# Optimization experiments

Hardware: AMD Instinct MI355X
Metric: run time of the kernel (lower is better)

Reference implementation:

```python
import jax, jax.numpy as jnp
import numpy as np

N, D_IN, D_OUT, Q_DIM = 4096, 256, 256, 64


def _xavier(key, shape):
    fan_in, fan_out = shape[-2], shape[-1]
    bound = float(np.sqrt(6.0 / (fan_in + fan_out)))
    return jax.random.uniform(key, shape, jnp.float32, -bound, bound)


def setup_inputs() -> dict:
    key = jax.random.key(0)
    k_x, k_q, k_w, k_b = jax.random.split(key, 4)
    x = jax.random.normal(k_x, (N, D_IN), jnp.float32)
    query_vectors = jax.random.normal(k_q, (N, Q_DIM), jnp.float32)
    W_1 = _xavier(k_w, (Q_DIM, D_IN, D_OUT))  # xavier over last two dims (matches torch on 3D)
    b_1 = _xavier(k_b, (Q_DIM, D_OUT))
    return {"x": x, "query_vectors": query_vectors, "W_1": W_1, "b_1": b_1}


def reference(x, query_vectors, W_1, b_1):
    # Per-sample dynamic weight: W[n] = sum_d q[n,d] * W_1[d]; then x[n] @ W[n] + q[n] @ b_1.
    # Fused single contraction avoids materializing the [n, i, o] tensor; same math.
    out = jnp.einsum('ni,nd,dio->no', x, query_vectors, W_1)
    out = out + query_vectors @ b_1
    return out
```

## Files before the change

kernel.cpp:

```cpp
#include <hip/hip_runtime.h>
#include <stdint.h>


typedef _Float16 f16;
typedef f16 f16x8 __attribute__((ext_vector_type(8)));
typedef float f32x16 __attribute__((ext_vector_type(16)));

#define QDIM 64

#define XFRAG(DST, PTR)                                      \
  do {                                                       \
    float4 a_ = *(const float4*)(PTR);                       \
    float4 b_ = *(const float4*)((PTR) + 4);                 \
    f16x8 h_;                                                \
    h_[0] = (f16)a_.x; h_[1] = (f16)a_.y; h_[2] = (f16)a_.z; \
    h_[3] = (f16)a_.w; h_[4] = (f16)b_.x; h_[5] = (f16)b_.y; \
    h_[6] = (f16)b_.z; h_[7] = (f16)b_.w;                    \
    DST = h_;                                                \
  } while (0)

__global__ __launch_bounds__(256) void prep(const float* __restrict__ W,
                                            const float* __restrict__ B1,
                                            const float* __restrict__ X,
                                            f16* __restrict__ Wt,
                                            f16* __restrict__ Xt,
                                            f16* __restrict__ Bt) {
  const int b = blockIdx.x, t = threadIdx.x;
  if (b < 512) {
    const int d = b >> 3, grp = b & 7;
#pragma unroll
    for (int r = 0; r < 4; ++r) {
      const int ib = (grp << 2) + r;
      const float* src = W + ((size_t)d * 256 + ((size_t)ib << 3)) * 256 + t;
      f16x8 h;
#pragma unroll
      for (int j = 0; j < 8; ++j) h[j] = (f16)src[(size_t)j << 8];
      const int nc = t >> 5, c = t & 31, ic = ib >> 1, hb = ib & 1;
      *(f16x8*)((char*)Wt + ((((size_t)nc * 64 + d) * 16 + ic) << 10) +
                (hb << 9) + (c << 4)) = h;
    }
  } else if (b < 576) {
    const int mb = b - 512;
#pragma unroll
    for (int rep = 0; rep < 8; ++rep) {
      const int u = (rep << 8) + t;
      const int row = u & 63, ish = u >> 6;
      const float* src = X + ((size_t)((mb << 6) + row)) * 256 + (ish << 3);
      f16x8 h;
      XFRAG(h, src);
      *(f16x8*)((char*)Xt + ((((size_t)mb * 16 + (ish >> 1)) * 2 + (ish & 1)) << 10) +
                (row << 4)) = h;
    }
  } else {
#pragma unroll
    for (int kb = 0; kb < 8; ++kb) {
      const float* src = B1 + ((size_t)kb << 3) * 256 + t;
      f16x8 h;
#pragma unroll
      for (int j = 0; j < 8; ++j) h[j] = (f16)src[(size_t)j << 8];
      *(f16x8*)((char*)Bt + (((size_t)(t >> 5) * 4 + (kb >> 1)) << 10) +
                ((kb & 1) << 9) + ((t & 31) << 4)) = h;
    }
  }
}

#define LOADX(D, IC)                                             \
  do {                                                           \
    D[0] = *(const f16x8*)(xb + ((size_t)(IC) << 11));           \
    D[1] = *(const f16x8*)(xb + ((size_t)(IC) << 11) + 512);     \
  } while (0)

#define FULL16(XF, ICN)                                                          \
  do {                                                                          \
    _Pragma("unroll")                                                           \
    for (int dq = 0; dq < 16; ++dq) {                                           \
      f16x8 wfr = Wr[dq];                                                       \
      Wr[dq] = *(const f16x8*)(wl + (((size_t)dq * 16 + (ICN)) << 10));         \
      f16x8 a0 = XF[0] * qr0[dq];                                               \
      acc0[dq & 1] = __builtin_amdgcn_mfma_f32_32x32x16_f16(                    \
          a0, wfr, acc0[dq & 1], 0, 0, 0);                                      \
      f16x8 a1 = XF[1] * qr1[dq];                                               \
      acc1[dq & 1] = __builtin_amdgcn_mfma_f32_32x32x16_f16(                    \
          a1, wfr, acc1[dq & 1], 0, 0, 0);                                      \
    }                                                                           \
  } while (0)

__global__ __launch_bounds__(256, 2) void mlp_main(const float* __restrict__ Q,
                                                   const f16* __restrict__ Wt,
                                                   const f16* __restrict__ Xt,
                                                   const f16* __restrict__ Bt,
                                                   float* __restrict__ out) {
  __shared__ __align__(16) float red[4][64][36];

  const int bid = blockIdx.x;
  const int nc = bid & 7;
  const int mb = bid >> 3;
  const int t = threadIdx.x;
  const int w = t >> 6;
  const int l = t & 63;
  const int l31 = l & 31;
  const int hf = l >> 5;

  const char* wl = (const char*)Wt + (((size_t)(nc * 64 + (w << 4))) << 14) +
                   (hf << 9) + (l31 << 4);
  const char* xb = (const char*)Xt + ((size_t)mb << 15) + (hf << 10) + (l31 << 4);

  f16 qr0[16], qr1[16];
  {
    const float* qp0 = Q + ((size_t)((mb << 6) + l31)) * QDIM + (w << 4);
    const float* qp1 = qp0 + (size_t)32 * QDIM;
#pragma unroll
    for (int g = 0; g < 4; ++g) {
      float4 v0 = *(const float4*)(qp0 + (g << 2));
      float4 v1 = *(const float4*)(qp1 + (g << 2));
      qr0[g * 4 + 0] = (f16)v0.x; qr0[g * 4 + 1] = (f16)v0.y;
      qr0[g * 4 + 2] = (f16)v0.z; qr0[g * 4 + 3] = (f16)v0.w;
      qr1[g * 4 + 0] = (f16)v1.x; qr1[g * 4 + 1] = (f16)v1.y;
      qr1[g * 4 + 2] = (f16)v1.z; qr1[g * 4 + 3] = (f16)v1.w;
    }
  }

  f32x16 acc0[2], acc1[2];
#pragma unroll
  for (int p = 0; p < 2; ++p)
#pragma unroll
    for (int r = 0; r < 16; ++r) { acc0[p][r] = 0.f; acc1[p][r] = 0.f; }

  f16x8 Wr[16], xfA[2], xfB[2];

  const int icoff = (mb & 7) << 1;

  LOADX(xfA, icoff);
#pragma unroll
  for (int dq = 0; dq < 16; ++dq)
    Wr[dq] = *(const f16x8*)(wl + (((size_t)dq * 16 + icoff) << 10));

  for (int ic2 = 0; ic2 < 8; ++ic2) {
    const int o  = ((ic2 << 1) + 1 + icoff) & 15;
    const int n2 = ((ic2 << 1) + 2 + icoff) & 15;
    LOADX(xfB, o);
    FULL16(xfA, o);
    LOADX(xfA, n2);
    FULL16(xfB, n2);
  }

#pragma unroll
  for (int r = 0; r < 16; ++r) {
    acc0[0][r] += acc0[1][r];
    acc1[0][r] += acc1[1][r];
  }

  if (w == 0) {
#pragma unroll
    for (int kc = 0; kc < 4; ++kc) {
      f16x8 bf = *(const f16x8*)((const char*)Bt +
          (((size_t)nc * 4 + kc) << 10) + (hf << 9) + (l31 << 4));
      f16x8 q0, q1;
      XFRAG(q0, Q + ((size_t)((mb << 6) + l31)) * QDIM + (kc << 4) + (hf << 3));
      XFRAG(q1, Q + ((size_t)((mb << 6) + 32 + l31)) * QDIM + (kc << 4) + (hf << 3));
      acc0[0] = __builtin_amdgcn_mfma_f32_32x32x16_f16(q0, bf, acc0[0], 0, 0, 0);
      acc1[0] = __builtin_amdgcn_mfma_f32_32x32x16_f16(q1, bf, acc1[0], 0, 0, 0);
    }
  }

#pragma unroll
  for (int r = 0; r < 16; ++r) {
    const int row0 = (r & 3) + ((r >> 2) << 3) + (hf << 2);
    red[w][row0][l31] = acc0[0][r];
    red[w][32 + row0][l31] = acc1[0][r];
  }
  __syncthreads();

  const int row = t >> 2;
  const int cq = (t & 3) << 3;
  float s[8];
#pragma unroll
  for (int j = 0; j < 8; ++j) s[j] = 0.f;
#pragma unroll
  for (int wq = 0; wq < 4; ++wq) {
    const float* rp = &red[wq][row][cq];
    float4 v0 = *(const float4*)rp;
    float4 v1 = *(const float4*)(rp + 4);
    s[0] += v0.x; s[1] += v0.y; s[2] += v0.z; s[3] += v0.w;
    s[4] += v1.x; s[5] += v1.y; s[6] += v1.z; s[7] += v1.w;
  }
  float4 o0 = {s[0], s[1], s[2], s[3]};
  float4 o1 = {s[4], s[5], s[6], s[7]};
  float* op = out + ((size_t)((mb << 6) + row)) * 256 + (nc << 5) + cq;
  *(float4*)op = o0;
  *(float4*)(op + 4) = o1;
}

extern "C" void kernel_launch(void* const* d_in, const int* in_sizes, int n_in,
                              void* d_out, int out_size, void* d_ws, size_t ws_size,
                              hipStream_t stream) {
  (void)in_sizes; (void)n_in; (void)out_size; (void)ws_size;
  const float* x  = (const float*)d_in[0];
  const float* q  = (const float*)d_in[1];
  const float* W1 = (const float*)d_in[2];
  const float* b1 = (const float*)d_in[3];
  float* out = (float*)d_out;

  f16* Wt = (f16*)d_ws;
  f16* Bt = (f16*)((char*)d_ws + ((size_t)8 << 20));
  f16* Xt = (f16*)((char*)d_ws + ((size_t)8 << 20) + 32768);

  prep<<<577, 256, 0, stream>>>(W1, b1, x, Wt, Xt, Bt);
  mlp_main<<<512, 256, 0, stream>>>(q, Wt, Xt, Bt, out);
}
```

Before: 120.6 us.

## Halve rows per block, double grid and occupancy; vectorize W prep loads

The main kernel now processes 32 rows per block instead of 64, launching 1024 blocks with a launch bound allowing 4 blocks per SM. The W register buffer is halved to 8 fragments, with a two-phase rotating prefetch over the 16 q-dimension slices, to cut register pressure and raise occupancy. The prep kernel now reads W with float4 loads per thread and transposes in registers to improve coalescing. In exchange, each W fragment loaded from memory is reused across half as many rows, doubling total W traffic from L2.

After: 133.1 us. 1.1x slower.

```diff
diff --git a/kernel.cpp b/kernel.cpp
--- a/kernel.cpp
+++ b/kernel.cpp
@@ -28,15 +28,24 @@
   const int b = blockIdx.x, t = threadIdx.x;
   if (b < 512) {
     const int d = b >> 3, grp = b & 7;
+    const int ibL = t >> 6;
+    const int ib = (grp << 2) + ibL;
+    const int o0 = (t & 63) << 2;
+    const int ic = ib >> 1, hb = ib & 1;
+    float v[32];
 #pragma unroll
-    for (int r = 0; r < 4; ++r) {
-      const int ib = (grp << 2) + r;
-      const float* src = W + ((size_t)d * 256 + ((size_t)ib << 3)) * 256 + t;
+    for (int j = 0; j < 8; ++j) {
+      float4 f = *(const float4*)(W + ((size_t)d * 256 + (ib << 3) + j) * 256 + o0);
+      v[j * 4 + 0] = f.x; v[j * 4 + 1] = f.y;
+      v[j * 4 + 2] = f.z; v[j * 4 + 3] = f.w;
+    }
+#pragma unroll
+    for (int oo = 0; oo < 4; ++oo) {
+      const int o = o0 + oo, ncb = o >> 5, c = o & 31;
       f16x8 h;
 #pragma unroll
-      for (int j = 0; j < 8; ++j) h[j] = (f16)src[(size_t)j << 8];
-      const int nc = t >> 5, c = t & 31, ic = ib >> 1, hb = ib & 1;
-      *(f16x8*)((char*)Wt + ((((size_t)nc * 64 + d) * 16 + ic) << 10) +
+      for (int j = 0; j < 8; ++j) h[j] = (f16)v[j * 4 + oo];
+      *(f16x8*)((char*)Wt + ((((size_t)ncb * 64 + d) * 16 + ic) << 10) +
                 (hb << 9) + (c << 4)) = h;
     }
   } else if (b < 576) {
@@ -64,33 +73,12 @@
   }
 }
 
-#define LOADX(D, IC)                                             \
-  do {                                                           \
-    D[0] = *(const f16x8*)(xb + ((size_t)(IC) << 11));           \
-    D[1] = *(const f16x8*)(xb + ((size_t)(IC) << 11) + 512);     \
-  } while (0)
-
-#define FULL16(XF, ICN)                                                          \
-  do {                                                                          \
-    _Pragma("unroll")                                                           \
-    for (int dq = 0; dq < 16; ++dq) {                                           \
-      f16x8 wfr = Wr[dq];                                                       \
-      Wr[dq] = *(const f16x8*)(wl + (((size_t)dq * 16 + (ICN)) << 10));         \
-      f16x8 a0 = XF[0] * qr0[dq];                                               \
-      acc0[dq & 1] = __builtin_amdgcn_mfma_f32_32x32x16_f16(                    \
-          a0, wfr, acc0[dq & 1], 0, 0, 0);                                      \
-      f16x8 a1 = XF[1] * qr1[dq];                                               \
-      acc1[dq & 1] = __builtin_amdgcn_mfma_f32_32x32x16_f16(                    \
-          a1, wfr, acc1[dq & 1], 0, 0, 0);                                      \
-    }                                                                           \
-  } while (0)
-
-__global__ __launch_bounds__(256, 2) void mlp_main(const float* __restrict__ Q,
+__global__ __launch_bounds__(256, 4) void mlp_main(const float* __restrict__ Q,
                                                    const f16* __restrict__ Wt,
                                                    const f16* __restrict__ Xt,
                                                    const f16* __restrict__ Bt,
                                                    float* __restrict__ out) {
-  __shared__ __align__(16) float red[4][64][36];
+  __shared__ __align__(16) float red[4][32][36];
 
   const int bid = blockIdx.x;
   const int nc = bid & 7;
@@ -103,92 +91,86 @@
 
   const char* wl = (const char*)Wt + (((size_t)(nc * 64 + (w << 4))) << 14) +
                    (hf << 9) + (l31 << 4);
-  const char* xb = (const char*)Xt + ((size_t)mb << 15) + (hf << 10) + (l31 << 4);
+  const char* xb = (const char*)Xt + ((size_t)(mb >> 1) << 15) + (hf << 10) +
+                   ((size_t)(((mb & 1) << 5) + l31) << 4);
 
-  f16 qr0[16], qr1[16];
+  f16 qr[16];
   {
-    const float* qp0 = Q + ((size_t)((mb << 6) + l31)) * QDIM + (w << 4);
-    const float* qp1 = qp0 + (size_t)32 * QDIM;
+    const float* qp = Q + ((size_t)((mb << 5) + l31)) * QDIM + (w << 4);
 #pragma unroll
     for (int g = 0; g < 4; ++g) {
-      float4 v0 = *(const float4*)(qp0 + (g << 2));
-      float4 v1 = *(const float4*)(qp1 + (g << 2));
-      qr0[g * 4 + 0] = (f16)v0.x; qr0[g * 4 + 1] = (f16)v0.y;
-      qr0[g * 4 + 2] = (f16)v0.z; qr0[g * 4 + 3] = (f16)v0.w;
-      qr1[g * 4 + 0] = (f16)v1.x; qr1[g * 4 + 1] = (f16)v1.y;
-      qr1[g * 4 + 2] = (f16)v1.z; qr1[g * 4 + 3] = (f16)v1.w;
+      float4 v = *(const float4*)(qp + (g << 2));
+      qr[g * 4 + 0] = (f16)v.x; qr[g * 4 + 1] = (f16)v.y;
+      qr[g * 4 + 2] = (f16)v.z; qr[g * 4 + 3] = (f16)v.w;
     }
   }
 
-  f32x16 acc0[2], acc1[2];
+  f32x16 acc[2];
 #pragma unroll
   for (int p = 0; p < 2; ++p)
 #pragma unroll
-    for (int r = 0; r < 16; ++r) { acc0[p][r] = 0.f; acc1[p][r] = 0.f; }
+    for (int r = 0; r < 16; ++r) acc[p][r] = 0.f;
 
-  f16x8 Wr[16], xfA[2], xfB[2];
+  f16x8 Wr[8], xfA, xfB;
 
-  const int icoff = (mb & 7) << 1;
+  const int icoff = (((mb & 7) << 1) | (((mb >> 5) & 1) << 3)) & 15;
 
-  LOADX(xfA, icoff);
+  xfA = *(const f16x8*)(xb + ((size_t)icoff << 11));
 #pragma unroll
-  for (int dq = 0; dq < 16; ++dq)
-    Wr[dq] = *(const f16x8*)(wl + (((size_t)dq * 16 + icoff) << 10));
+  for (int i = 0; i < 8; ++i)
+    Wr[i] = *(const f16x8*)(wl + (((size_t)(i * 16 + icoff)) << 10));
 
-  for (int ic2 = 0; ic2 < 8; ++ic2) {
-    const int o  = ((ic2 << 1) + 1 + icoff) & 15;
-    const int n2 = ((ic2 << 1) + 2 + icoff) & 15;
-    LOADX(xfB, o);
-    FULL16(xfA, o);
-    LOADX(xfA, n2);
-    FULL16(xfB, n2);
+  for (int s = 0; s < 16; ++s) {
+    const int ic = (icoff + s) & 15;
+    const int icn = (icoff + s + 1) & 15;
+    xfB = *(const f16x8*)(xb + ((size_t)icn << 11));
+#pragma unroll
+    for (int i = 0; i < 8; ++i) {
+      f16x8 wfr = Wr[i];
+      Wr[i] = *(const f16x8*)(wl + (((size_t)((8 + i) * 16 + ic)) << 10));
+      f16x8 a = xfA * qr[i];
+      acc[i & 1] = __builtin_amdgcn_mfma_f32_32x32x16_f16(a, wfr, acc[i & 1], 0, 0, 0);
+    }
+#pragma unroll
+    for (int i = 0; i < 8; ++i) {
+      f16x8 wfr = Wr[i];
+      Wr[i] = *(const f16x8*)(wl + (((size_t)(i * 16 + icn)) << 10));
+      f16x8 a = xfA * qr[8 + i];
+      acc[i & 1] = __builtin_amdgcn_mfma_f32_32x32x16_f16(a, wfr, acc[i & 1], 0, 0, 0);
+    }
+    xfA = xfB;
   }
 
 #pragma unroll
-  for (int r = 0; r < 16; ++r) {
-    acc0[0][r] += acc0[1][r];
-    acc1[0][r] += acc1[1][r];
-  }
+  for (int r = 0; r < 16; ++r) acc[0][r] += acc[1][r];
 
   if (w == 0) {
 #pragma unroll
     for (int kc = 0; kc < 4; ++kc) {
       f16x8 bf = *(const f16x8*)((const char*)Bt +
           (((size_t)nc * 4 + kc) << 10) + (hf << 9) + (l31 << 4));
-      f16x8 q0, q1;
-      XFRAG(q0, Q + ((size_t)((mb << 6) + l31)) * QDIM + (kc << 4) + (hf << 3));
-      XFRAG(q1, Q + ((size_t)((mb << 6) + 32 + l31)) * QDIM + (kc << 4) + (hf << 3));
-      acc0[0] = __builtin_amdgcn_mfma_f32_32x32x16_f16(q0, bf, acc0[0], 0, 0, 0);
-      acc1[0] = __builtin_amdgcn_mfma_f32_32x32x16_f16(q1, bf, acc1[0], 0, 0, 0);
+      f16x8 q0;
+      XFRAG(q0, Q + ((size_t)((mb << 5) + l31)) * QDIM + (kc << 4) + (hf << 3));
+      acc[0] = __builtin_amdgcn_mfma_f32_32x32x16_f16(q0, bf, acc[0], 0, 0, 0);
     }
   }
 
 #pragma unroll
   for (int r = 0; r < 16; ++r) {
     const int row0 = (r & 3) + ((r >> 2) << 3) + (hf << 2);
-    red[w][row0][l31] = acc0[0][r];
-    red[w][32 + row0][l31] = acc1[0][r];
+    red[w][row0][l31] = acc[0][r];
   }
   __syncthreads();
 
-  const int row = t >> 2;
-  const int cq = (t & 3) << 3;
-  float s[8];
-#pragma unroll
-  for (int j = 0; j < 8; ++j) s[j] = 0.f;
+  const int row = t >> 3;
+  const int cg = (t & 7) << 2;
+  float4 sum = {0.f, 0.f, 0.f, 0.f};
 #pragma unroll
   for (int wq = 0; wq < 4; ++wq) {
-    const float* rp = &red[wq][row][cq];
-    float4 v0 = *(const float4*)rp;
-    float4 v1 = *(const float4*)(rp + 4);
-    s[0] += v0.x; s[1] += v0.y; s[2] += v0.z; s[3] += v0.w;
-    s[4] += v1.x; s[5] += v1.y; s[6] += v1.z; s[7] += v1.w;
+    float4 v = *(const float4*)(&red[wq][row][cg]);
+    sum.x += v.x; sum.y += v.y; sum.z += v.z; sum.w += v.w;
   }
-  float4 o0 = {s[0], s[1], s[2], s[3]};
-  float4 o1 = {s[4], s[5], s[6], s[7]};
-  float* op = out + ((size_t)((mb << 6) + row)) * 256 + (nc << 5) + cq;
-  *(float4*)op = o0;
-  *(float4*)(op + 4) = o1;
+  *(float4*)(out + ((size_t)((mb << 5) + row)) * 256 + (nc << 5) + cg) = sum;
 }
 
 extern "C" void kernel_launch(void* const* d_in, const int* in_sizes, int n_in,
@@ -206,5 +188,5 @@
   f16* Xt = (f16*)((char*)d_ws + ((size_t)8 << 20) + 32768);
 
   prep<<<577, 256, 0, stream>>>(W1, b1, x, Wt, Xt, Bt);
-  mlp_main<<<512, 256, 0, stream>>>(q, Wt, Xt, Bt, out);
+  mlp_main<<<1024, 256, 0, stream>>>(q, Wt, Xt, Bt, out);
 }
```

## Retile main kernel to 128-row tiles with split-K halves and LDS-staged X

Applied to the files above, without the earlier changes.

The main kernel now processes 128 rows per block with 8 waves, splitting the input dimension across two blocks (ksi) and writing partial sums to a workspace that a new reduce2 kernel adds together. X fragments are staged into LDS via global_load_lds, and each W fragment feeds four MFMAs instead of two, which improves W reuse. The cost is an extra kernel launch, a 2x4MB partial-output round trip, larger LDS use, and a two-phase in-block reduction.

Result: slower. 150.6 us (+24.9%).

```diff
diff --git a/kernel.cpp b/kernel.cpp
--- a/kernel.cpp
+++ b/kernel.cpp
@@ -7,6 +7,13 @@
 typedef float f32x16 __attribute__((ext_vector_type(16)));
 
 #define QDIM 64
+
+__device__ __forceinline__ void gl_lds16(const void* g, void* s) {
+  __builtin_amdgcn_global_load_lds(
+      (const __attribute__((address_space(1))) void*)(uintptr_t)g,
+      (__attribute__((address_space(3))) void*)(uint32_t)(uintptr_t)s,
+      16, 0, 0);
+}
 
 #define XFRAG(DST, PTR)                                      \
   do {                                                       \
@@ -30,13 +37,16 @@
     const int d = b >> 3, grp = b & 7;
 #pragma unroll
     for (int r = 0; r < 4; ++r) {
-      const int ib = (grp << 2) + r;
-      const float* src = W + ((size_t)d * 256 + ((size_t)ib << 3)) * 256 + t;
+      const int u = (r << 8) + t;
+      const int ibq = u >> 8;
+      const int o = u & 255;
+      const int ib = (grp << 2) + ibq;
       f16x8 h;
 #pragma unroll
-      for (int j = 0; j < 8; ++j) h[j] = (f16)src[(size_t)j << 8];
-      const int nc = t >> 5, c = t & 31, ic = ib >> 1, hb = ib & 1;
-      *(f16x8*)((char*)Wt + ((((size_t)nc * 64 + d) * 16 + ic) << 10) +
+      for (int j = 0; j < 8; ++j)
+        h[j] = (f16)W[((size_t)d * 256 + (ib << 3) + j) * 256 + o];
+      const int ncg = o >> 5, c = o & 31, ic = ib >> 1, hb = ib & 1;
+      *(f16x8*)((char*)Wt + ((((size_t)ncg * 64 + d) * 16 + ic) << 10) +
                 (hb << 9) + (c << 4)) = h;
     }
   } else if (b < 576) {
@@ -64,121 +74,146 @@
   }
 }
 
-#define LOADX(D, IC)                                             \
-  do {                                                           \
-    D[0] = *(const f16x8*)(xb + ((size_t)(IC) << 11));           \
-    D[1] = *(const f16x8*)(xb + ((size_t)(IC) << 11) + 512);     \
-  } while (0)
-
-#define FULL16(XF, ICN)                                                          \
-  do {                                                                          \
-    _Pragma("unroll")                                                           \
-    for (int dq = 0; dq < 16; ++dq) {                                           \
-      f16x8 wfr = Wr[dq];                                                       \
-      Wr[dq] = *(const f16x8*)(wl + (((size_t)dq * 16 + (ICN)) << 10));         \
-      f16x8 a0 = XF[0] * qr0[dq];                                               \
-      acc0[dq & 1] = __builtin_amdgcn_mfma_f32_32x32x16_f16(                    \
-          a0, wfr, acc0[dq & 1], 0, 0, 0);                                      \
-      f16x8 a1 = XF[1] * qr1[dq];                                               \
-      acc1[dq & 1] = __builtin_amdgcn_mfma_f32_32x32x16_f16(                    \
-          a1, wfr, acc1[dq & 1], 0, 0, 0);                                      \
-    }                                                                           \
-  } while (0)
-
-__global__ __launch_bounds__(256, 2) void mlp_main(const float* __restrict__ Q,
+__global__ __launch_bounds__(512, 4) void mlp_main(const float* __restrict__ Q,
                                                    const f16* __restrict__ Wt,
                                                    const f16* __restrict__ Xt,
                                                    const f16* __restrict__ Bt,
-                                                   float* __restrict__ out) {
-  __shared__ __align__(16) float red[4][64][36];
+                                                   float* __restrict__ P) {
+  __shared__ __align__(16) char smem[73728];
 
   const int bid = blockIdx.x;
   const int nc = bid & 7;
-  const int mb = bid >> 3;
+  const int ksi = (bid >> 3) & 1;
+  const int mb = bid >> 4;
   const int t = threadIdx.x;
   const int w = t >> 6;
   const int l = t & 63;
   const int l31 = l & 31;
   const int hf = l >> 5;
-
-  const char* wl = (const char*)Wt + (((size_t)(nc * 64 + (w << 4))) << 14) +
-                   (hf << 9) + (l31 << 4);
-  const char* xb = (const char*)Xt + ((size_t)mb << 15) + (hf << 10) + (l31 << 4);
-
-  f16 qr0[16], qr1[16];
-  {
-    const float* qp0 = Q + ((size_t)((mb << 6) + l31)) * QDIM + (w << 4);
-    const float* qp1 = qp0 + (size_t)32 * QDIM;
-#pragma unroll
-    for (int g = 0; g < 4; ++g) {
-      float4 v0 = *(const float4*)(qp0 + (g << 2));
-      float4 v1 = *(const float4*)(qp1 + (g << 2));
-      qr0[g * 4 + 0] = (f16)v0.x; qr0[g * 4 + 1] = (f16)v0.y;
-      qr0[g * 4 + 2] = (f16)v0.z; qr0[g * 4 + 3] = (f16)v0.w;
-      qr1[g * 4 + 0] = (f16)v1.x; qr1[g * 4 + 1] = (f16)v1.y;
-      qr1[g * 4 + 2] = (f16)v1.z; qr1[g * 4 + 3] = (f16)v1.w;
-    }
-  }
-
-  f32x16 acc0[2], acc1[2];
-#pragma unroll
-  for (int p = 0; p < 2; ++p)
-#pragma unroll
-    for (int r = 0; r < 16; ++r) { acc0[p][r] = 0.f; acc1[p][r] = 0.f; }
-
-  f16x8 Wr[16], xfA[2], xfB[2];
-
-  const int icoff = (mb & 7) << 1;
-
-  LOADX(xfA, icoff);
-#pragma unroll
-  for (int dq = 0; dq < 16; ++dq)
-    Wr[dq] = *(const f16x8*)(wl + (((size_t)dq * 16 + icoff) << 10));
-
-  for (int ic2 = 0; ic2 < 8; ++ic2) {
-    const int o  = ((ic2 << 1) + 1 + icoff) & 15;
-    const int n2 = ((ic2 << 1) + 2 + icoff) & 15;
-    LOADX(xfB, o);
-    FULL16(xfA, o);
-    LOADX(xfA, n2);
-    FULL16(xfB, n2);
-  }
-
-#pragma unroll
-  for (int r = 0; r < 16; ++r) {
-    acc0[0][r] += acc0[1][r];
-    acc1[0][r] += acc1[1][r];
-  }
-
-  if (w == 0) {
+  const int rot = mb & 7;
+
+  const char* wB = (const char*)Wt + ((size_t)nc << 20) + (w << 17) +
+                   (ksi << 13) + (l << 4);
+#define WADDR(S) \
+  (wB + ((((((S) & 7) + rot) & 7)) << 14) + ((((S) >> 3)) << 10))
+
+  f16x8 qv[4];
+#pragma unroll
+  for (int mt = 0; mt < 4; ++mt) {
+    const float* qp = Q + ((size_t)((mb << 7) + (mt << 5) + l31)) * QDIM + (w << 3);
+#pragma unroll
+    for (int dt = 0; dt < 8; ++dt) qv[mt][dt] = (f16)qp[(dt + rot) & 7];
+  }
+
+  f16x8 Wr0 = *(const f16x8*)WADDR(0);
+  f16x8 Wr1 = *(const f16x8*)WADDR(1);
+  f16x8 Wr2 = *(const f16x8*)WADDR(2);
+  f16x8 Wr3 = *(const f16x8*)WADDR(3);
+
+#pragma unroll
+  for (int r = 0; r < 4; ++r) {
+    const int t64 = (r >> 1) & 1, half = r & 1;
+    const char* src = (const char*)Xt +
+        ((((size_t)((mb << 1) + t64) << 4) + (ksi << 3) + w) << 11) +
+        (half << 10) + (l << 4);
+    gl_lds16(src, smem + ((((w << 2) + r)) << 10) + (l << 4));
+  }
+
+  f32x16 acc0, acc1, acc2, acc3;
+#pragma unroll
+  for (int r = 0; r < 16; ++r) { acc0[r] = 0.f; acc1[r] = 0.f;
+                                 acc2[r] = 0.f; acc3[r] = 0.f; }
+
+  __syncthreads();
+
+  f16x8 xf0, xf1, xf2, xf3;
+#define LOADXF(IC)                                                          \
+  do {                                                                      \
+    const char* xb_ = smem + ((IC) << 12) + (hf << 10) + (l31 << 4);        \
+    xf0 = *(const f16x8*)(xb_);                                             \
+    xf1 = *(const f16x8*)(xb_ + 512);                                       \
+    xf2 = *(const f16x8*)(xb_ + 2048);                                      \
+    xf3 = *(const f16x8*)(xb_ + 2560);                                      \
+  } while (0)
+
+#define STEP(S, WR)                                                         \
+  do {                                                                      \
+    f16x8 wf_ = WR;                                                         \
+    if ((S) < 60) WR = *(const f16x8*)WADDR((S) + 4);                       \
+    acc0 = __builtin_amdgcn_mfma_f32_32x32x16_f16(xf0 * qv[0][(S) & 7],     \
+                                                  wf_, acc0, 0, 0, 0);      \
+    acc1 = __builtin_amdgcn_mfma_f32_32x32x16_f16(xf1 * qv[1][(S) & 7],     \
+                                                  wf_, acc1, 0, 0, 0);      \
+    acc2 = __builtin_amdgcn_mfma_f32_32x32x16_f16(xf2 * qv[2][(S) & 7],     \
+                                                  wf_, acc2, 0, 0, 0);      \
+    acc3 = __builtin_amdgcn_mfma_f32_32x32x16_f16(xf3 * qv[3][(S) & 7],     \
+                                                  wf_, acc3, 0, 0, 0);      \
+  } while (0)
+
+#pragma unroll
+  for (int ic = 0; ic < 8; ++ic) {
+    LOADXF(ic);
+    STEP(ic * 8 + 0, Wr0);
+    STEP(ic * 8 + 1, Wr1);
+    STEP(ic * 8 + 2, Wr2);
+    STEP(ic * 8 + 3, Wr3);
+    STEP(ic * 8 + 4, Wr0);
+    STEP(ic * 8 + 5, Wr1);
+    STEP(ic * 8 + 6, Wr2);
+    STEP(ic * 8 + 7, Wr3);
+  }
+
+  if (ksi == 0 && w == 7) {
 #pragma unroll
     for (int kc = 0; kc < 4; ++kc) {
       f16x8 bf = *(const f16x8*)((const char*)Bt +
           (((size_t)nc * 4 + kc) << 10) + (hf << 9) + (l31 << 4));
-      f16x8 q0, q1;
-      XFRAG(q0, Q + ((size_t)((mb << 6) + l31)) * QDIM + (kc << 4) + (hf << 3));
-      XFRAG(q1, Q + ((size_t)((mb << 6) + 32 + l31)) * QDIM + (kc << 4) + (hf << 3));
-      acc0[0] = __builtin_amdgcn_mfma_f32_32x32x16_f16(q0, bf, acc0[0], 0, 0, 0);
-      acc1[0] = __builtin_amdgcn_mfma_f32_32x32x16_f16(q1, bf, acc1[0], 0, 0, 0);
-    }
-  }
-
-#pragma unroll
-  for (int r = 0; r < 16; ++r) {
-    const int row0 = (r & 3) + ((r >> 2) << 3) + (hf << 2);
-    red[w][row0][l31] = acc0[0][r];
-    red[w][32 + row0][l31] = acc1[0][r];
+      f16x8 q0, q1, q2, q3;
+      XFRAG(q0, Q + ((size_t)((mb << 7) + l31)) * QDIM + (kc << 4) + (hf << 3));
+      XFRAG(q1, Q + ((size_t)((mb << 7) + 32 + l31)) * QDIM + (kc << 4) + (hf << 3));
+      XFRAG(q2, Q + ((size_t)((mb << 7) + 64 + l31)) * QDIM + (kc << 4) + (hf << 3));
+      XFRAG(q3, Q + ((size_t)((mb << 7) + 96 + l31)) * QDIM + (kc << 4) + (hf << 3));
+      acc0 = __builtin_amdgcn_mfma_f32_32x32x16_f16(q0, bf, acc0, 0, 0, 0);
+      acc1 = __builtin_amdgcn_mfma_f32_32x32x16_f16(q1, bf, acc1, 0, 0, 0);
+      acc2 = __builtin_amdgcn_mfma_f32_32x32x16_f16(q2, bf, acc2, 0, 0, 0);
+      acc3 = __builtin_amdgcn_mfma_f32_32x32x16_f16(q3, bf, acc3, 0, 0, 0);
+    }
+  }
+
+#define RED(WQ, ROW, COL) \
+  (((float*)smem)[(((WQ) * 128 + (ROW)) * 36) + (COL)])
+  __syncthreads();
+  if (w < 4) {
+#pragma unroll
+    for (int r = 0; r < 16; ++r) {
+      const int rr = (r & 3) + ((r >> 2) << 3) + (hf << 2);
+      RED(w, rr, l31) = acc0[r];
+      RED(w, 32 + rr, l31) = acc1[r];
+      RED(w, 64 + rr, l31) = acc2[r];
+      RED(w, 96 + rr, l31) = acc3[r];
+    }
+  }
+  __syncthreads();
+  if (w >= 4) {
+#pragma unroll
+    for (int r = 0; r < 16; ++r) {
+      const int rr = (r & 3) + ((r >> 2) << 3) + (hf << 2);
+      RED(w - 4, rr, l31) += acc0[r];
+      RED(w - 4, 32 + rr, l31) += acc1[r];
+      RED(w - 4, 64 + rr, l31) += acc2[r];
+      RED(w - 4, 96 + rr, l31) += acc3[r];
+    }
   }
   __syncthreads();
 
   const int row = t >> 2;
-  const int cq = (t & 3) << 3;
+  const int c0 = (t & 3) << 3;
   float s[8];
 #pragma unroll
   for (int j = 0; j < 8; ++j) s[j] = 0.f;
 #pragma unroll
-  for (int wq = 0; wq < 4; ++wq) {
-    const float* rp = &red[wq][row][cq];
+  for (int j = 0; j < 4; ++j) {
+    const float* rp = &RED(j, row, c0);
     float4 v0 = *(const float4*)rp;
     float4 v1 = *(const float4*)(rp + 4);
     s[0] += v0.x; s[1] += v0.y; s[2] += v0.z; s[3] += v0.w;
@@ -186,9 +221,19 @@
   }
   float4 o0 = {s[0], s[1], s[2], s[3]};
   float4 o1 = {s[4], s[5], s[6], s[7]};
-  float* op = out + ((size_t)((mb << 6) + row)) * 256 + (nc << 5) + cq;
+  float* op = P + ((size_t)ksi << 20) +
+              ((size_t)((mb << 7) + row)) * 256 + (nc << 5) + c0;
   *(float4*)op = o0;
   *(float4*)(op + 4) = o1;
+}
+
+__global__ __launch_bounds__(256) void reduce2(const float* __restrict__ P,
+                                               float* __restrict__ out) {
+  const size_t i = (((size_t)blockIdx.x << 8) + threadIdx.x) << 2;
+  float4 a = *(const float4*)(P + i);
+  float4 b = *(const float4*)(P + ((size_t)1 << 20) + i);
+  a.x += b.x; a.y += b.y; a.z += b.z; a.w += b.w;
+  *(float4*)(out + i) = a;
 }
 
 extern "C" void kernel_launch(void* const* d_in, const int* in_sizes, int n_in,
@@ -204,7 +249,9 @@
   f16* Wt = (f16*)d_ws;
   f16* Bt = (f16*)((char*)d_ws + ((size_t)8 << 20));
   f16* Xt = (f16*)((char*)d_ws + ((size_t)8 << 20) + 32768);
+  float* P = (float*)((char*)d_ws + ((size_t)8 << 20) + 32768 + ((size_t)2 << 20));
 
   prep<<<577, 256, 0, stream>>>(W1, b1, x, Wt, Xt, Bt);
-  mlp_main<<<512, 256, 0, stream>>>(q, Wt, Xt, Bt, out);
-}
+  mlp_main<<<512, 512, 0, stream>>>(q, Wt, Xt, Bt, P);
+  reduce2<<<1024, 256, 0, stream>>>(P, out);
+}
```
